# Kernel optimization log

Measured on AMD Instinct MI355X. Metric: run time of the kernel, lower is better.

The kernel has to match this reference:

```python
import jax, jax.numpy as jnp
import numpy as np

N_UE = 16384
N_AP = 128
E = 2097152
D = 32

relu = jax.nn.relu


def setup_inputs():
    key = jax.random.key(0)
    ks = jax.random.split(key, 24)
    def g(i, shape, s=0.1):
        return jax.random.normal(ks[i], shape, dtype=jnp.float32) * s
    inp = {}
    inp["x_ue"] = jax.random.uniform(ks[0], (N_UE, 1), dtype=jnp.float32)
    inp["e_ua"] = g(1, (E, 2), 1.0)
    inp["e_au"] = g(2, (E, 2), 1.0)
    inp["src"] = jax.random.randint(ks[3], (E,), 0, N_UE)
    inp["dst"] = jax.random.randint(ks[4], (E,), 0, N_AP)
    # layer 1 (Ue2Ap): ue feat dim 1, ap feat dim 0, edge dim 2
    inp["Wm1_ua"] = g(5, (1 + 2, D)); inp["bm1_ua"] = jnp.zeros((D,), jnp.float32)
    inp["Wm1_au"] = g(6, (2, D));     inp["bm1_au"] = jnp.zeros((D,), jnp.float32)
    inp["Wu1_ap"] = g(7, (D, D));     inp["bu1_ap"] = jnp.zeros((D,), jnp.float32)
    inp["Wu1_ue"] = g(8, (1 + D, D)); inp["bu1_ue"] = jnp.zeros((D,), jnp.float32)
    inp["We1_ua"] = g(9, (2 * D + 2, 2));  inp["be1_ua"] = jnp.zeros((2,), jnp.float32)
    inp["We1_au"] = g(10, (2 * D + 2, 2)); inp["be1_au"] = jnp.zeros((2,), jnp.float32)
    # layers 2-4 stacked (all 32 -> 32)
    inp["Wm_ua"] = g(11, (3, D + 2, D)); inp["bm_ua"] = jnp.zeros((3, D), jnp.float32)
    inp["Wm_au"] = g(12, (3, D + 2, D)); inp["bm_au"] = jnp.zeros((3, D), jnp.float32)
    inp["Wu_ap"] = g(13, (3, 2 * D, D)); inp["bu_ap"] = jnp.zeros((3, D), jnp.float32)
    inp["Wu_ue"] = g(14, (3, 2 * D, D)); inp["bu_ue"] = jnp.zeros((3, D), jnp.float32)
    inp["We_ua"] = g(15, (3, 2 * D + 2, 2)); inp["be_ua"] = jnp.zeros((3, 2), jnp.float32)
    inp["We_au"] = g(16, (3, 2 * D + 2, 2)); inp["be_au"] = jnp.zeros((3, 2), jnp.float32)
    # power head: mlp([32,16]) + Lin(16,1) + Sigmoid
    inp["Wp1"] = g(17, (D, 16)); inp["bp1"] = jnp.zeros((16,), jnp.float32)
    inp["Wp2"] = g(18, (16, 1)); inp["bp2"] = jnp.zeros((1,), jnp.float32)
    return inp


def _het_conv(x_ue, x_ap, e_ua, e_au, src, dst,
              Wm_ua, bm_ua, Wm_au, bm_au,
              Wu_ap, bu_ap, Wu_ue, bu_ue,
              We_ua, be_ua, We_au, be_au):
    # ue -> ap: gather src ue feats + edge attr, MLP, scatter-add to ap
    f_ua = jnp.concatenate([x_ue[src], e_ua], axis=1)        # [E, d_ue+2]
    m_ua = relu(f_ua @ Wm_ua + bm_ua)                        # [E, D]
    agg_ap = jax.ops.segment_sum(m_ua, dst, num_segments=N_AP)
    # ap -> ue: ap has no features in layer 1 (dim 0)
    f_au = e_au if x_ap is None else jnp.concatenate([x_ap[dst], e_au], axis=1)
    m_au = relu(f_au @ Wm_au + bm_au)                        # [E, D]
    agg_ue = jax.ops.segment_sum(m_au, src, num_segments=N_UE)
    # node updates
    h_ap = agg_ap if x_ap is None else jnp.concatenate([x_ap, agg_ap], axis=1)
    x_ap_new = relu(h_ap @ Wu_ap + bu_ap)                    # [N_AP, D]
    x_ue_new = relu(jnp.concatenate([x_ue, agg_ue], axis=1) @ Wu_ue + bu_ue)  # [N_UE, D]
    # edge updates (keep edge_dim = 2)
    pair = jnp.concatenate([x_ue_new[src], x_ap_new[dst]], axis=1)  # [E, 2D]
    e_ua_new = relu(jnp.concatenate([pair, e_ua], axis=1) @ We_ua + be_ua)
    e_au_new = relu(jnp.concatenate([pair, e_au], axis=1) @ We_au + be_au)
    return x_ue_new, x_ap_new, e_ua_new, e_au_new


def reference(x_ue, e_ua, e_au, src, dst,
              Wm1_ua, bm1_ua, Wm1_au, bm1_au, Wu1_ap, bu1_ap, Wu1_ue, bu1_ue,
              We1_ua, be1_ua, We1_au, be1_au,
              Wm_ua, bm_ua, Wm_au, bm_au, Wu_ap, bu_ap, Wu_ue, bu_ue,
              We_ua, be_ua, We_au, be_au,
              Wp1, bp1, Wp2, bp2):
    x_ue, x_ap, e_ua, e_au = _het_conv(
        x_ue, None, e_ua, e_au, src, dst,
        Wm1_ua, bm1_ua, Wm1_au, bm1_au, Wu1_ap, bu1_ap, Wu1_ue, bu1_ue,
        We1_ua, be1_ua, We1_au, be1_au)
    for l in range(3):  # conv2, conv3, conv4
        x_ue, x_ap, e_ua, e_au = _het_conv(
            x_ue, x_ap, e_ua, e_au, src, dst,
            Wm_ua[l], bm_ua[l], Wm_au[l], bm_au[l],
            Wu_ap[l], bu_ap[l], Wu_ue[l], bu_ue[l],
            We_ua[l], be_ua[l], We_au[l], be_au[l])
    power = jax.nn.sigmoid(relu(x_ue @ Wp1 + bp1) @ Wp2 + bp2)  # [N_UE, 1]
    ue_out = jnp.concatenate([x_ue[:, :1], power], axis=1)      # [N_UE, 2]
    return ue_out, x_ap, e_ua, e_au
```

## Files before the change

### kernel.cpp

```cpp
#include <hip/hip_runtime.h>
#include <math.h>

#define N_UE 16384
#define N_AP 128
#define NE   2097152
#define NSB  256
#define EPSB (NE / NSB)
#define NHALF (N_UE / 2)
#define CHS  8
#define CHD  16
#define NEP  (NE + CHS * N_UE)
#define NCHU (NEP / CHS)
#define NEPD (NE + CHD * N_AP)
#define NCHD_AL 131328
#define SRC_BLKS (NCHU / 256)
#define DST_BLKS (NCHD_AL / 256)

#define RFL(x) __int_as_float(__builtin_amdgcn_readfirstlane(__float_as_int(x)))

__global__ __launch_bounds__(256) void prefill(
    int* __restrict__ dtS, int* __restrict__ srcD,
    int* __restrict__ cnS, int* __restrict__ cnD)
{
    int i = blockIdx.x * 256 + threadIdx.x;
    dtS[i] = N_AP;
    if (i < NEPD) srcD[i] = N_UE;
    if (i < NCHU) cnS[i] = -1;
    if (i < NCHD_AL) cnD[i] = -1;
}

__global__ __launch_bounds__(256) void init_kernel(
    const float* __restrict__ x_ue, const float* __restrict__ Wm1_ua,
    const float* __restrict__ bm1_ua, const float* __restrict__ bm1_au,
    float* __restrict__ Qua, float* __restrict__ Pau)
{
    int i = blockIdx.x * 256 + threadIdx.x;
    int d = i & 31;
    Qua[i] = fmaf(x_ue[i >> 5], Wm1_ua[d], bm1_ua[d]);
    if (i < N_AP * 32) Pau[i] = bm1_au[d];
    if (i < 32) { Qua[N_UE * 32 + i] = -1e30f; Pau[N_AP * 32 + i] = -1e30f; }
}

__global__ __launch_bounds__(256) void hist_both(
    const int* __restrict__ src, const int* __restrict__ dst,
    unsigned short* __restrict__ histS, int* __restrict__ histD)
{
    __shared__ unsigned int h32[N_UE / 2];
    __shared__ int hd[N_AP];
    const int tid = threadIdx.x, b = blockIdx.x;
    for (int i = tid; i < N_UE / 2; i += 256) h32[i] = 0u;
    if (tid < N_AP) hd[tid] = 0;
    __syncthreads();
    const int beg = b * EPSB;
    for (int e = beg + tid; e < beg + EPSB; e += 256) {
        int s = src[e];
        atomicAdd(&h32[s >> 1], 1u << ((s & 1) * 16));
        atomicAdd(&hd[dst[e]], 1);
    }
    __syncthreads();
    for (int i = tid; i < N_UE; i += 256)
        histS[(size_t)b * N_UE + i] =
            (unsigned short)((h32[i >> 1] >> ((i & 1) * 16)) & 0xffffu);
    if (tid < N_AP) histD[b * N_AP + tid] = hd[tid];
}

__global__ __launch_bounds__(256) void colscan_kernel(
    const unsigned short* __restrict__ histS,
    unsigned short* __restrict__ baseS, int* __restrict__ cnt)
{
    const int u = blockIdx.x * 256 + threadIdx.x;
    int run = 0;
    for (int b = 0; b < NSB; ++b) {
        int t = histS[(size_t)b * N_UE + u];
        baseS[(size_t)b * N_UE + u] = (unsigned short)run;
        run += t;
    }
    cnt[u] = run;
}

__global__ __launch_bounds__(256) void scan_src(
    const int* __restrict__ cnt, int* __restrict__ CU)
{
    __shared__ int ps[256];
    __shared__ int ps2[257];
    const int t = threadIdx.x;
    const int b0 = t * (N_UE / 256);
    int s = 0;
    for (int i = 0; i < N_UE / 256; ++i) s += (cnt[b0 + i] + CHS - 1) / CHS;
    ps[t] = s;
    __syncthreads();
    if (t == 0) {
        int r = 0;
        for (int i = 0; i < 256; ++i) { ps2[i] = r; r += ps[i]; }
        ps2[256] = r;
    }
    __syncthreads();
    int r = ps2[t];
    for (int i = 0; i < N_UE / 256; ++i) { CU[b0 + i] = r; r += (cnt[b0 + i] + CHS - 1) / CHS; }
    if (t == 255) CU[N_UE] = ps2[256];
}

__global__ __launch_bounds__(128) void scan_dst(
    const int* __restrict__ histD, int* __restrict__ offsD, int* __restrict__ CA)
{
    __shared__ int colTot[N_AP], colStart[N_AP];
    const int a = threadIdx.x;
    int run = 0;
    for (int b = 0; b < NSB; ++b) {
        offsD[b * N_AP + a] = run;
        run += histD[b * N_AP + a];
    }
    colTot[a] = run;
    __syncthreads();
    if (a == 0) {
        int r = 0;
        for (int i = 0; i < N_AP; ++i) {
            CA[i] = r;
            colStart[i] = r * CHD;
            r += (colTot[i] + CHD - 1) / CHD;
        }
        CA[N_AP] = r;
    }
    __syncthreads();
    const int st = colStart[a];
    for (int b = 0; b < NSB; ++b) offsD[b * N_AP + a] += st;
}

__global__ __launch_bounds__(256) void scatter_both(
    const int* __restrict__ src, const int* __restrict__ dst,
    const float2* __restrict__ e0ua, const float2* __restrict__ e0au,
    const unsigned short* __restrict__ baseS, const int* __restrict__ CU,
    const int* __restrict__ offsD,
    int* __restrict__ dtS, float2* __restrict__ attS, int* __restrict__ invS,
    int* __restrict__ srcD, float2* __restrict__ attD, int* __restrict__ invD)
{
    __shared__ int cursor[NHALF];
    __shared__ int cursord[N_AP];
    const int tid = threadIdx.x, b = blockIdx.x;
    const int beg = b * EPSB;
    if (tid < N_AP) cursord[tid] = offsD[b * N_AP + tid];
    for (int p = 0; p < 2; ++p) {
        const int lo = p * NHALF;
        for (int i = tid; i < NHALF; i += 256)
            cursor[i] = CU[lo + i] * CHS + (int)baseS[(size_t)b * N_UE + lo + i];
        __syncthreads();
        for (int e = beg + tid; e < beg + EPSB; e += 256) {
            int s = src[e];
            int dt = dst[e];
            if (p == 0) {
                int posd = atomicAdd(&cursord[dt], 1);
                srcD[posd] = s;
                attD[posd] = e0ua[e];
                invD[e] = posd;
            }
            if (s >= lo && s < lo + NHALF) {
                int pos = atomicAdd(&cursor[s - lo], 1);
                dtS[pos] = dt;
                attS[pos] = e0au[e];
                invS[e] = pos;
            }
        }
        __syncthreads();
    }
}

__global__ __launch_bounds__(256) void build_map_src(
    const int* __restrict__ CU, int* __restrict__ cnS)
{
    const int u = blockIdx.x * 256 + threadIdx.x;
    const int c0 = CU[u], c1 = CU[u + 1];
    for (int c = c0; c < c1; ++c) cnS[c] = u;
}

__global__ __launch_bounds__(128) void build_map_dst(
    const int* __restrict__ CA, int* __restrict__ cnD)
{
    const int a = threadIdx.x;
    const int c0 = CA[a], c1 = CA[a + 1];
    for (int c = c0; c < c1; ++c) cnD[c] = a;
}

template<bool EUPD>
__global__ __launch_bounds__(256) void pass_both(
    const int* __restrict__ cnS, const int* __restrict__ dtS,
    float2* __restrict__ attS,
    const int* __restrict__ cnD, const int* __restrict__ srcD,
    float2* __restrict__ attD,
    const float2* __restrict__ RueA, const float2* __restrict__ RueB,
    const float2* __restrict__ RapA, const float2* __restrict__ RapB,
    const float* __restrict__ EcA, const float* __restrict__ EcB,
    const float* __restrict__ Qua, const float* __restrict__ Pau,
    const float* __restrict__ cu, const float* __restrict__ cw,
    float* __restrict__ partialU, float* __restrict__ partialA)
{
    if (blockIdx.x < SRC_BLKS) {
        const int ch = blockIdx.x * 256 + threadIdx.x;
        const int u = cnS[ch];
        if (u < 0) return;
        float w0v[32], w1v[32];
        #pragma unroll
        for (int d = 0; d < 32; ++d) { w0v[d] = RFL(cw[d]); w1v[d] = RFL(cw[32 + d]); }
        float d00 = 0.f, d01 = 0.f, d10 = 0.f, d11 = 0.f, rbx = 0.f, rby = 0.f;
        if constexpr (EUPD) {
            d00 = RFL(EcB[0]); d01 = RFL(EcB[1]); d10 = RFL(EcB[2]); d11 = RFL(EcB[3]);
            float2 r = RueB[u]; rbx = r.x; rby = r.y;
        }
        const float4* __restrict__ Pau4 = (const float4*)Pau;
        const int base = ch * CHS;
        float4 acc[8];
        #pragma unroll
        for (int q = 0; q < 8; ++q) acc[q] = make_float4(0.f, 0.f, 0.f, 0.f);
        #pragma unroll
        for (int j = 0; j < CHS; ++j) {
            int dt = dtS[base + j];
            float2 a = attS[base + j];
            if constexpr (EUPD) {
                float2 rp = RapB[dt];
                float m0 = fmaxf(rbx + rp.x + a.x * d00 + a.y * d10, 0.f);
                float m1 = fmaxf(rby + rp.y + a.x * d01 + a.y * d11, 0.f);
                a = make_float2(m0, m1);
                attS[base + j] = a;
            }
            const float4* pr = Pau4 + dt * 8;
            #pragma unroll
            for (int q = 0; q < 8; ++q) {
                float4 pv = pr[q];
                acc[q].x += fmaxf(fmaf(a.x, w0v[q*4+0], fmaf(a.y, w1v[q*4+0], pv.x)), 0.f);
                acc[q].y += fmaxf(fmaf(a.x, w0v[q*4+1], fmaf(a.y, w1v[q*4+1], pv.y)), 0.f);
                acc[q].z += fmaxf(fmaf(a.x, w0v[q*4+2], fmaf(a.y, w1v[q*4+2], pv.z)), 0.f);
                acc[q].w += fmaxf(fmaf(a.x, w0v[q*4+3], fmaf(a.y, w1v[q*4+3], pv.w)), 0.f);
            }
        }
        float4* pu = (float4*)(partialU + (size_t)ch * 32);
        #pragma unroll
        for (int q = 0; q < 8; ++q) pu[q] = acc[q];
    } else {
        const int ch = (blockIdx.x - SRC_BLKS) * 256 + threadIdx.x;
        const int a = cnD[ch];
        if (a < 0) return;
        float u0v[32], u1v[32];
        #pragma unroll
        for (int d = 0; d < 32; ++d) { u0v[d] = RFL(cu[d]); u1v[d] = RFL(cu[32 + d]); }
        float c00 = 0.f, c01 = 0.f, c10 = 0.f, c11 = 0.f, rax = 0.f, ray = 0.f;
        if constexpr (EUPD) {
            c00 = RFL(EcA[0]); c01 = RFL(EcA[1]); c10 = RFL(EcA[2]); c11 = RFL(EcA[3]);
            float2 r = RapA[a]; rax = r.x; ray = r.y;
        }
        const float4* __restrict__ Qua4 = (const float4*)Qua;
        const int base = ch * CHD;
        float4 acc[8];
        #pragma unroll
        for (int q = 0; q < 8; ++q) acc[q] = make_float4(0.f, 0.f, 0.f, 0.f);
        #pragma unroll 4
        for (int j = 0; j < CHD; ++j) {
            int s = srcD[base + j];
            float2 a2 = attD[base + j];
            if constexpr (EUPD) {
                float2 ru = RueA[s];
                float n0 = fmaxf(rax + ru.x + a2.x * c00 + a2.y * c10, 0.f);
                float n1 = fmaxf(ray + ru.y + a2.x * c01 + a2.y * c11, 0.f);
                a2 = make_float2(n0, n1);
                attD[base + j] = a2;
            }
            const float4* qr = Qua4 + s * 8;
            #pragma unroll
            for (int q = 0; q < 8; ++q) {
                float4 qv = qr[q];
                acc[q].x += fmaxf(fmaf(a2.x, u0v[q*4+0], fmaf(a2.y, u1v[q*4+0], qv.x)), 0.f);
                acc[q].y += fmaxf(fmaf(a2.x, u0v[q*4+1], fmaf(a2.y, u1v[q*4+1], qv.y)), 0.f);
                acc[q].z += fmaxf(fmaf(a2.x, u0v[q*4+2], fmaf(a2.y, u1v[q*4+2], qv.z)), 0.f);
                acc[q].w += fmaxf(fmaf(a2.x, u0v[q*4+3], fmaf(a2.y, u1v[q*4+3], qv.w)), 0.f);
            }
        }
        float4* pa = (float4*)(partialA + (size_t)ch * 32);
        #pragma unroll
        for (int q = 0; q < 8; ++q) pa[q] = acc[q];
    }
}

__global__ __launch_bounds__(256) void reduce_ue(
    const int* __restrict__ CU, const float* __restrict__ partialU,
    float* __restrict__ agg_ue)
{
    const int g   = (blockIdx.x * 256 + threadIdx.x) >> 5;
    const int dim = threadIdx.x & 31;
    const int c0 = CU[g], c1 = CU[g + 1];
    float acc = 0.f;
    for (int c = c0; c < c1; ++c) acc += partialU[(size_t)c * 32 + dim];
    agg_ue[g * 32 + dim] = acc;
}

__global__ __launch_bounds__(256) void final_edge(
    const int* __restrict__ src, const int* __restrict__ dst,
    const int* __restrict__ invS, const int* __restrict__ invD,
    const float2* __restrict__ attS, const float2* __restrict__ attD,
    const float2* __restrict__ RueA, const float2* __restrict__ RueB,
    const float2* __restrict__ RapA, const float2* __restrict__ RapB,
    const float* __restrict__ EcA, const float* __restrict__ EcB,
    float2* __restrict__ out_eua, float2* __restrict__ out_eau)
{
    const int e = blockIdx.x * 256 + threadIdx.x;
    const int s = src[e], dt = dst[e];
    float c00 = EcA[0], c01 = EcA[1], c10 = EcA[2], c11 = EcA[3];
    float d00 = EcB[0], d01 = EcB[1], d10 = EcB[2], d11 = EcB[3];
    float2 eua = attD[invD[e]];
    float2 eau = attS[invS[e]];
    float2 rA = RueA[s], pA = RapA[dt];
    float n0 = fmaxf(rA.x + pA.x + eua.x * c00 + eua.y * c10, 0.f);
    float n1 = fmaxf(rA.y + pA.y + eua.x * c01 + eua.y * c11, 0.f);
    float2 rB = RueB[s], pB = RapB[dt];
    float m0 = fmaxf(rB.x + pB.x + eau.x * d00 + eau.y * d10, 0.f);
    float m1 = fmaxf(rB.y + pB.y + eau.x * d01 + eau.y * d11, 0.f);
    out_eua[e] = make_float2(n0, n1);
    out_eau[e] = make_float2(m0, m1);
}

template<bool FIRST, bool LAST>
__global__ __launch_bounds__(64) void node_ue_kernel(
    const float* __restrict__ x_prev, const float* __restrict__ agg_ue,
    const float* __restrict__ Wu, const float* __restrict__ bu,
    const float* __restrict__ Wm_next, const float* __restrict__ bm_next,
    const float* __restrict__ WeUa, const float* __restrict__ WeUb,
    const float* __restrict__ Wp1, const float* __restrict__ bp1,
    const float* __restrict__ Wp2, const float* __restrict__ bp2,
    float* __restrict__ x_new, float* __restrict__ Qua_next,
    float2* __restrict__ RueA, float2* __restrict__ RueB,
    float2* __restrict__ ue_out)
{
    constexpr int KIN = FIRST ? 33 : 64;
    __shared__ float Wu_s[64 * 32];
    __shared__ float Wm_s[32 * 32];
    __shared__ float WeA_s[64], WeB_s[64];
    __shared__ float bu_s[32], bm_s[32];
    __shared__ float Wp1_s[32 * 16], bp1_s[16], Wp2_s[16];

    const int tid = threadIdx.x;
    for (int i = tid; i < KIN * 32; i += 64) Wu_s[i] = Wu[i];
    if (tid < 32) bu_s[tid] = bu[tid];
    if (!LAST) {
        for (int i = tid; i < 1024; i += 64) Wm_s[i] = Wm_next[i];
        if (tid < 32) bm_s[tid] = bm_next[tid];
    }
    { WeA_s[tid] = WeUa[tid]; WeB_s[tid] = WeUb[tid]; }
    if (LAST) {
        for (int i = tid; i < 512; i += 64) Wp1_s[i] = Wp1[i];
        if (tid < 16) { bp1_s[tid] = bp1[tid]; Wp2_s[tid] = Wp2[tid]; }
    }
    __syncthreads();

    const int u = blockIdx.x * 64 + tid;
    float in[KIN];
    if (FIRST) {
        in[0] = x_prev[u];
        #pragma unroll
        for (int k = 0; k < 32; ++k) in[1 + k] = agg_ue[u * 32 + k];
    } else {
        #pragma unroll
        for (int k = 0; k < 32; ++k) in[k] = x_prev[u * 32 + k];
        #pragma unroll
        for (int k = 0; k < 32; ++k) in[32 + k] = agg_ue[u * 32 + k];
    }
    float out[32];
    #pragma unroll
    for (int d = 0; d < 32; ++d) {
        float acc = bu_s[d];
        #pragma unroll
        for (int k = 0; k < KIN; ++k) acc = fmaf(in[k], Wu_s[k * 32 + d], acc);
        out[d] = fmaxf(acc, 0.f);
    }
    #pragma unroll
    for (int d = 0; d < 32; ++d) x_new[u * 32 + d] = out[d];
    if (!LAST) {
        #pragma unroll
        for (int d = 0; d < 32; ++d) {
            float acc = bm_s[d];
            #pragma unroll
            for (int k = 0; k < 32; ++k) acc = fmaf(out[k], Wm_s[k * 32 + d], acc);
            Qua_next[u * 32 + d] = acc;
        }
    }
    float r0 = 0.f, r1 = 0.f, s0 = 0.f, s1 = 0.f;
    #pragma unroll
    for (int k = 0; k < 32; ++k) {
        r0 = fmaf(out[k], WeA_s[k * 2],     r0);
        r1 = fmaf(out[k], WeA_s[k * 2 + 1], r1);
        s0 = fmaf(out[k], WeB_s[k * 2],     s0);
        s1 = fmaf(out[k], WeB_s[k * 2 + 1], s1);
    }
    RueA[u] = make_float2(r0, r1);
    RueB[u] = make_float2(s0, s1);
    if (LAST) {
        float z = bp2[0];
        #pragma unroll
        for (int j = 0; j < 16; ++j) {
            float h = bp1_s[j];
            #pragma unroll
            for (int k = 0; k < 32; ++k) h = fmaf(out[k], Wp1_s[k * 16 + j], h);
// ... 47 lines not shown
        float xn = fmaxf(acc2, 0.f);
        xnew_s[d] = xn;
        x_new[a * 32 + d] = xn;
    }
    __syncthreads();
    if (!LAST) {
        if (tid < 32) {
            float acc3 = bm_next[d];
            #pragma unroll
            for (int k = 0; k < 32; ++k) acc3 = fmaf(xnew_s[k], Wm_next[k * 32 + d], acc3);
            Pau_next[a * 32 + d] = acc3;
        }
    }
    if (tid == 0) {
        float q0 = beA[0], q1 = beA[1], t0 = beB[0], t1 = beB[1];
        #pragma unroll
        for (int k = 0; k < 32; ++k) {
            q0 = fmaf(xnew_s[k], WeA[k * 2],     q0);
            q1 = fmaf(xnew_s[k], WeA[k * 2 + 1], q1);
            t0 = fmaf(xnew_s[k], WeB[k * 2],     t0);
            t1 = fmaf(xnew_s[k], WeB[k * 2 + 1], t1);
        }
        RapA[a] = make_float2(q0, q1);
        RapB[a] = make_float2(t0, t1);
    }
}

extern "C" void kernel_launch(void* const* d_in, const int* in_sizes, int n_in,
                              void* d_out_v, int out_size, void* d_ws, size_t ws_size,
                              hipStream_t stream)
{
    const float*  x_ue   = (const float*)d_in[0];
    const float2* e0ua   = (const float2*)d_in[1];
    const float2* e0au   = (const float2*)d_in[2];
    const int*    src    = (const int*)d_in[3];
    const int*    dst    = (const int*)d_in[4];
    const float* Wm1_ua = (const float*)d_in[5];
    const float* bm1_ua = (const float*)d_in[6];
    const float* Wm1_au = (const float*)d_in[7];
    const float* bm1_au = (const float*)d_in[8];
    const float* Wu1_ap = (const float*)d_in[9];
    const float* bu1_ap = (const float*)d_in[10];
    const float* Wu1_ue = (const float*)d_in[11];
    const float* bu1_ue = (const float*)d_in[12];
    const float* We1_ua = (const float*)d_in[13];
    const float* be1_ua = (const float*)d_in[14];
    const float* We1_au = (const float*)d_in[15];
    const float* be1_au = (const float*)d_in[16];
    const float* Wm_ua  = (const float*)d_in[17];
    const float* bm_ua  = (const float*)d_in[18];
    const float* Wm_au  = (const float*)d_in[19];
    const float* bm_au  = (const float*)d_in[20];
    const float* Wu_ap  = (const float*)d_in[21];
    const float* bu_ap  = (const float*)d_in[22];
    const float* Wu_ue  = (const float*)d_in[23];
    const float* bu_ue  = (const float*)d_in[24];
    const float* We_ua  = (const float*)d_in[25];
    const float* be_ua  = (const float*)d_in[26];
    const float* We_au  = (const float*)d_in[27];
    const float* be_au  = (const float*)d_in[28];
    const float* Wp1    = (const float*)d_in[29];
    const float* bp1    = (const float*)d_in[30];
    const float* Wp2    = (const float*)d_in[31];
    const float* bp2    = (const float*)d_in[32];

    float*  outp    = (float*)d_out_v;
    float2* out_ue  = (float2*)outp;
    float*  out_ap  = outp + N_UE * 2;
    float2* out_eua = (float2*)(outp + N_UE * 2 + N_AP * 32);
    float2* out_eau = (float2*)(outp + N_UE * 2 + N_AP * 32 + (size_t)NE * 2);

    float* ws = (float*)d_ws;
    float* x_ueA  = ws;          ws += N_UE * 32;
    float* x_ueB  = ws;          ws += N_UE * 32;
    float* x_apA  = ws;          ws += N_AP * 32;
    float* x_apB  = ws;          ws += N_AP * 32;
    float* agg_ue = ws;          ws += N_UE * 32;
    float* Qua    = ws;          ws += (N_UE + 1) * 32;
    float* Pau    = ws;          ws += (N_AP + 1) * 32;
    float2* RueA  = (float2*)ws; ws += (N_UE + 2) * 2;
    float2* RueB  = (float2*)ws; ws += (N_UE + 2) * 2;
    float2* RapA  = (float2*)ws; ws += (N_AP + 2) * 2;
    float2* RapB  = (float2*)ws; ws += (N_AP + 2) * 2;
    int* cnt   = (int*)ws;       ws += N_UE;
    int* CU    = (int*)ws;       ws += N_UE + 4;
    int* histD = (int*)ws;       ws += NSB * N_AP;
    int* offsD = (int*)ws;       ws += NSB * N_AP;
    int* CA    = (int*)ws;       ws += N_AP + 4;
    int* cnS   = (int*)ws;       ws += NCHU;
    int* cnD   = (int*)ws;       ws += NCHD_AL;
    int* invS  = (int*)ws;       ws += NE;
    int* invD  = (int*)ws;       ws += NE;
    int* dtS   = (int*)ws;       ws += NEP;
    int* srcD  = (int*)ws;       ws += NEPD;
    float2* attS = (float2*)ws;  ws += (size_t)NEP * 2;
    float2* attD = (float2*)ws;  ws += (size_t)NEPD * 2;
    float* partialU = ws;        ws += (size_t)NCHU * 32;
    float* partialA = ws;        ws += (size_t)NCHD_AL * 32;
    unsigned short* histS = (unsigned short*)partialU;
    unsigned short* baseS = (unsigned short*)(partialU + (size_t)(NSB * N_UE / 2));

    dim3 blk(256);

    prefill<<<NEP / 256, blk, 0, stream>>>(dtS, srcD, cnS, cnD);
    hist_both<<<NSB, blk, 0, stream>>>(src, dst, histS, histD);
    colscan_kernel<<<N_UE / 256, blk, 0, stream>>>(histS, baseS, cnt);
    scan_src<<<1, blk, 0, stream>>>(cnt, CU);
    scan_dst<<<1, dim3(128), 0, stream>>>(histD, offsD, CA);
    scatter_both<<<NSB, blk, 0, stream>>>(src, dst, e0ua, e0au, baseS, CU, offsD,
                                          dtS, attS, invS, srcD, attD, invD);
    build_map_src<<<N_UE / 256, blk, 0, stream>>>(CU, cnS);
    build_map_dst<<<1, dim3(128), 0, stream>>>(CA, cnD);

    init_kernel<<<N_UE * 32 / 256, blk, 0, stream>>>(x_ue, Wm1_ua, bm1_ua, bm1_au, Qua, Pau);

    const int PB = SRC_BLKS + DST_BLKS;

    pass_both<false><<<PB, blk, 0, stream>>>(
        cnS, dtS, attS, cnD, srcD, attD,
        nullptr, nullptr, nullptr, nullptr, nullptr, nullptr,
        Qua, Pau, Wm1_ua + 32, Wm1_au, partialU, partialA);
    reduce_ue<<<N_UE * 32 / 256, blk, 0, stream>>>(CU, partialU, agg_ue);
    node_ue_kernel<true, false><<<N_UE / 64, dim3(64), 0, stream>>>(
        x_ue, agg_ue, Wu1_ue, bu1_ue, Wm_ua, bm_ua, We1_ua, We1_au,
        nullptr, nullptr, nullptr, nullptr,
        x_ueA, Qua, RueA, RueB, nullptr);
    node_ap_kernel<true, false><<<N_AP, blk, 0, stream>>>(
        partialA, CA, nullptr, Wu1_ap, bu1_ap, Wm_au, bm_au,
        We1_ua + 64, be1_ua, We1_au + 64, be1_au,
        x_apA, Pau, RapA, RapB);

    pass_both<true><<<PB, blk, 0, stream>>>(
        cnS, dtS, attS, cnD, srcD, attD,
        RueA, RueB, RapA, RapB, We1_ua + 128, We1_au + 128,
        Qua, Pau, Wm_ua + 1024, Wm_au + 1024, partialU, partialA);
    reduce_ue<<<N_UE * 32 / 256, blk, 0, stream>>>(CU, partialU, agg_ue);
    node_ue_kernel<false, false><<<N_UE / 64, dim3(64), 0, stream>>>(
        x_ueA, agg_ue, Wu_ue, bu_ue, Wm_ua + 1088, bm_ua + 32, We_ua, We_au,
        nullptr, nullptr, nullptr, nullptr,
        x_ueB, Qua, RueA, RueB, nullptr);
    node_ap_kernel<false, false><<<N_AP, blk, 0, stream>>>(
        partialA, CA, x_apA, Wu_ap, bu_ap, Wm_au + 1088, bm_au + 32,
        We_ua + 64, be_ua, We_au + 64, be_au,
        x_apB, Pau, RapA, RapB);

    pass_both<true><<<PB, blk, 0, stream>>>(
        cnS, dtS, attS, cnD, srcD, attD,
        RueA, RueB, RapA, RapB, We_ua + 128, We_au + 128,
        Qua, Pau, Wm_ua + 2112, Wm_au + 2112, partialU, partialA);
    reduce_ue<<<N_UE * 32 / 256, blk, 0, stream>>>(CU, partialU, agg_ue);
    node_ue_kernel<false, false><<<N_UE / 64, dim3(64), 0, stream>>>(
        x_ueB, agg_ue, Wu_ue + 2048, bu_ue + 32, Wm_ua + 2176, bm_ua + 64,
        We_ua + 132, We_au + 132,
        nullptr, nullptr, nullptr, nullptr,
        x_ueA, Qua, RueA, RueB, nullptr);
    node_ap_kernel<false, false><<<N_AP, blk, 0, stream>>>(
        partialA, CA, x_apB, Wu_ap + 2048, bu_ap + 32, Wm_au + 2176, bm_au + 64,
        We_ua + 196, be_ua + 2, We_au + 196, be_au + 2,
        x_apA, Pau, RapA, RapB);

    pass_both<true><<<PB, blk, 0, stream>>>(
        cnS, dtS, attS, cnD, srcD, attD,
        RueA, RueB, RapA, RapB, We_ua + 260, We_au + 260,
        Qua, Pau, Wm_ua + 3200, Wm_au + 3200, partialU, partialA);
    reduce_ue<<<N_UE * 32 / 256, blk, 0, stream>>>(CU, partialU, agg_ue);
    node_ue_kernel<false, true><<<N_UE / 64, dim3(64), 0, stream>>>(
        x_ueA, agg_ue, Wu_ue + 4096, bu_ue + 64, nullptr, nullptr,
        We_ua + 264, We_au + 264,
        Wp1, bp1, Wp2, bp2,
        x_ueB, nullptr, RueA, RueB, out_ue);
    node_ap_kernel<false, true><<<N_AP, blk, 0, stream>>>(
        partialA, CA, x_apA, Wu_ap + 4096, bu_ap + 64, nullptr, nullptr,
        We_ua + 328, be_ua + 4, We_au + 328, be_au + 4,
        out_ap, nullptr, RapA, RapB);

    final_edge<<<NE / 256, blk, 0, stream>>>(
        src, dst, invS, invD, attS, attD,
        RueA, RueB, RapA, RapB,
        We_ua + 392, We_au + 392, out_eua, out_eau);
}
```

Measured before the change: 891.9 us.

## Pack edge records into int4 AoS and scatter final edges by original index

Replaces the separate dst/attr/inverse-index arrays with a single 16-byte record per sorted edge (attr, neighbor, original edge id). The scatter becomes single-pass using packed 16-bit shared counters over all UEs, and NSB doubles while the src chunk size goes from 8 to 16. final_edge now walks the sorted records and writes outputs to the original edge slot, replacing the two indirect gathers through inverse indices with one scattered write. Records are wider, so each pass_both read moves more bytes, and the larger chunk size adds padding.

```diff
diff --git a/kernel.cpp b/kernel.cpp
--- a/kernel.cpp
+++ b/kernel.cpp
@@ -4,10 +4,9 @@
 #define N_UE 16384
 #define N_AP 128
 #define NE   2097152
-#define NSB  256
+#define NSB  512
 #define EPSB (NE / NSB)
-#define NHALF (N_UE / 2)
-#define CHS  8
+#define CHS  16
 #define CHD  16
 #define NEP  (NE + CHS * N_UE)
 #define NCHU (NEP / CHS)
@@ -19,12 +18,12 @@
 #define RFL(x) __int_as_float(__builtin_amdgcn_readfirstlane(__float_as_int(x)))
 
 __global__ __launch_bounds__(256) void prefill(
-    int* __restrict__ dtS, int* __restrict__ srcD,
+    int4* __restrict__ recS, int4* __restrict__ recD,
     int* __restrict__ cnS, int* __restrict__ cnD)
 {
     int i = blockIdx.x * 256 + threadIdx.x;
-    dtS[i] = N_AP;
-    if (i < NEPD) srcD[i] = N_UE;
+    recS[i] = make_int4(0, 0, N_AP, -1);
+    if (i < NEPD) recD[i] = make_int4(0, 0, N_UE, -1);
     if (i < NCHU) cnS[i] = -1;
     if (i < NCHD_AL) cnD[i] = -1;
 }
@@ -131,36 +130,25 @@
     const float2* __restrict__ e0ua, const float2* __restrict__ e0au,
     const unsigned short* __restrict__ baseS, const int* __restrict__ CU,
     const int* __restrict__ offsD,
-    int* __restrict__ dtS, float2* __restrict__ attS, int* __restrict__ invS,
-    int* __restrict__ srcD, float2* __restrict__ attD, int* __restrict__ invD)
-{
-    __shared__ int cursor[NHALF];
-    __shared__ int cursord[N_AP];
+    int4* __restrict__ recS, int4* __restrict__ recD)
+{
+    __shared__ unsigned int curS[N_UE / 2];
+    __shared__ int curD[N_AP];
     const int tid = threadIdx.x, b = blockIdx.x;
+    for (int i = tid; i < N_UE / 2; i += 256) curS[i] = 0u;
+    if (tid < N_AP) curD[tid] = offsD[b * N_AP + tid];
+    __syncthreads();
     const int beg = b * EPSB;
-    if (tid < N_AP) cursord[tid] = offsD[b * N_AP + tid];
-    for (int p = 0; p < 2; ++p) {
-        const int lo = p * NHALF;
-        for (int i = tid; i < NHALF; i += 256)
-            cursor[i] = CU[lo + i] * CHS + (int)baseS[(size_t)b * N_UE + lo + i];
-        __syncthreads();
-        for (int e = beg + tid; e < beg + EPSB; e += 256) {
-            int s = src[e];
-            int dt = dst[e];
-            if (p == 0) {
-                int posd = atomicAdd(&cursord[dt], 1);
-                srcD[posd] = s;
-                attD[posd] = e0ua[e];
-                invD[e] = posd;
-            }
-            if (s >= lo && s < lo + NHALF) {
-                int pos = atomicAdd(&cursor[s - lo], 1);
-                dtS[pos] = dt;
-                attS[pos] = e0au[e];
-                invS[e] = pos;
-            }
-        }
-        __syncthreads();
+    for (int e = beg + tid; e < beg + EPSB; e += 256) {
+        const int s = src[e], dt = dst[e];
+        unsigned int old = atomicAdd(&curS[s >> 1], 1u << ((s & 1) * 16));
+        int local = (int)((old >> ((s & 1) * 16)) & 0xffffu);
+        int pos = CU[s] * CHS + (int)baseS[(size_t)b * N_UE + s] + local;
+        float2 au = e0au[e];
+        recS[pos] = make_int4(__float_as_int(au.x), __float_as_int(au.y), dt, e);
+        int posd = atomicAdd(&curD[dt], 1);
+        float2 ua = e0ua[e];
+        recD[posd] = make_int4(__float_as_int(ua.x), __float_as_int(ua.y), s, e);
     }
 }
 
@@ -182,10 +170,8 @@
 
 template<bool EUPD>
 __global__ __launch_bounds__(256) void pass_both(
-    const int* __restrict__ cnS, const int* __restrict__ dtS,
-    float2* __restrict__ attS,
-    const int* __restrict__ cnD, const int* __restrict__ srcD,
-    float2* __restrict__ attD,
+    const int* __restrict__ cnS, int4* __restrict__ recS,
+    const int* __restrict__ cnD, int4* __restrict__ recD,
     const float2* __restrict__ RueA, const float2* __restrict__ RueB,
     const float2* __restrict__ RapA, const float2* __restrict__ RapB,
     const float* __restrict__ EcA, const float* __restrict__ EcB,
@@ -210,16 +196,17 @@
         float4 acc[8];
         #pragma unroll
         for (int q = 0; q < 8; ++q) acc[q] = make_float4(0.f, 0.f, 0.f, 0.f);
-        #pragma unroll
+        #pragma unroll 4
         for (int j = 0; j < CHS; ++j) {
-            int dt = dtS[base + j];
-            float2 a = attS[base + j];
+            int4 r4 = recS[base + j];
+            int dt = r4.z;
+            float2 a = make_float2(__int_as_float(r4.x), __int_as_float(r4.y));
             if constexpr (EUPD) {
                 float2 rp = RapB[dt];
                 float m0 = fmaxf(rbx + rp.x + a.x * d00 + a.y * d10, 0.f);
                 float m1 = fmaxf(rby + rp.y + a.x * d01 + a.y * d11, 0.f);
                 a = make_float2(m0, m1);
-                attS[base + j] = a;
+                *(float2*)&recS[base + j] = a;
             }
             const float4* pr = Pau4 + dt * 8;
             #pragma unroll
@@ -253,14 +240,15 @@
         for (int q = 0; q < 8; ++q) acc[q] = make_float4(0.f, 0.f, 0.f, 0.f);
         #pragma unroll 4
         for (int j = 0; j < CHD; ++j) {
-            int s = srcD[base + j];
-            float2 a2 = attD[base + j];
+            int4 r4 = recD[base + j];
+            int s = r4.z;
+            float2 a2 = make_float2(__int_as_float(r4.x), __int_as_float(r4.y));
             if constexpr (EUPD) {
                 float2 ru = RueA[s];
                 float n0 = fmaxf(rax + ru.x + a2.x * c00 + a2.y * c10, 0.f);
                 float n1 = fmaxf(ray + ru.y + a2.x * c01 + a2.y * c11, 0.f);
                 a2 = make_float2(n0, n1);
-                attD[base + j] = a2;
+                *(float2*)&recD[base + j] = a2;
             }
             const float4* qr = Qua4 + s * 8;
             #pragma unroll
@@ -291,28 +279,38 @@
 }
 
 __global__ __launch_bounds__(256) void final_edge(
-    const int* __restrict__ src, const int* __restrict__ dst,
-    const int* __restrict__ invS, const int* __restrict__ invD,
-    const float2* __restrict__ attS, const float2* __restrict__ attD,
+    const int4* __restrict__ recS, const int4* __restrict__ recD,
+    const int* __restrict__ cnS, const int* __restrict__ cnD,
     const float2* __restrict__ RueA, const float2* __restrict__ RueB,
     const float2* __restrict__ RapA, const float2* __restrict__ RapB,
     const float* __restrict__ EcA, const float* __restrict__ EcB,
     float2* __restrict__ out_eua, float2* __restrict__ out_eau)
 {
-    const int e = blockIdx.x * 256 + threadIdx.x;
-    const int s = src[e], dt = dst[e];
+    const int i = blockIdx.x * 256 + threadIdx.x;
     float c00 = EcA[0], c01 = EcA[1], c10 = EcA[2], c11 = EcA[3];
     float d00 = EcB[0], d01 = EcB[1], d10 = EcB[2], d11 = EcB[3];
-    float2 eua = attD[invD[e]];
-    float2 eau = attS[invS[e]];
-    float2 rA = RueA[s], pA = RapA[dt];
-    float n0 = fmaxf(rA.x + pA.x + eua.x * c00 + eua.y * c10, 0.f);
-    float n1 = fmaxf(rA.y + pA.y + eua.x * c01 + eua.y * c11, 0.f);
-    float2 rB = RueB[s], pB = RapB[dt];
-    float m0 = fmaxf(rB.x + pB.x + eau.x * d00 + eau.y * d10, 0.f);
-    float m1 = fmaxf(rB.y + pB.y + eau.x * d01 + eau.y * d11, 0.f);
-    out_eua[e] = make_float2(n0, n1);
-    out_eau[e] = make_float2(m0, m1);
+    {
+        int4 r = recS[i];
+        if (r.z != N_AP) {
+            const int u = cnS[i >> 4];
+            float2 a = make_float2(__int_as_float(r.x), __int_as_float(r.y));
+            float2 rB = RueB[u], pB = RapB[r.z];
+            float m0 = fmaxf(rB.x + pB.x + a.x * d00 + a.y * d10, 0.f);
+            float m1 = fmaxf(rB.y + pB.y + a.x * d01 + a.y * d11, 0.f);
+            out_eau[r.w] = make_float2(m0, m1);
+        }
+    }
+    if (i < NEPD) {
+        int4 r = recD[i];
+        if (r.z != N_UE) {
+            const int ap = cnD[i >> 4];
+            float2 a = make_float2(__int_as_float(r.x), __int_as_float(r.y));
+            float2 rA = RueA[r.z], pA = RapA[ap];
+            float n0 = fmaxf(rA.x + pA.x + a.x * c00 + a.y * c10, 0.f);
+            float n1 = fmaxf(rA.y + pA.y + a.x * c01 + a.y * c11, 0.f);
+            out_eua[r.w] = make_float2(n0, n1);
+        }
+    }
 }
 
 template<bool FIRST, bool LAST>
@@ -526,33 +524,29 @@
     float2* RueB  = (float2*)ws; ws += (N_UE + 2) * 2;
     float2* RapA  = (float2*)ws; ws += (N_AP + 2) * 2;
     float2* RapB  = (float2*)ws; ws += (N_AP + 2) * 2;
-    int* cnt   = (int*)ws;       ws += N_UE;
-    int* CU    = (int*)ws;       ws += N_UE + 4;
-    int* histD = (int*)ws;       ws += NSB * N_AP;
-    int* offsD = (int*)ws;       ws += NSB * N_AP;
-    int* CA    = (int*)ws;       ws += N_AP + 4;
-    int* cnS   = (int*)ws;       ws += NCHU;
-    int* cnD   = (int*)ws;       ws += NCHD_AL;
-    int* invS  = (int*)ws;       ws += NE;
-    int* invD  = (int*)ws;       ws += NE;
-    int* dtS   = (int*)ws;       ws += NEP;
-    int* srcD  = (int*)ws;       ws += NEPD;
-    float2* attS = (float2*)ws;  ws += (size_t)NEP * 2;
-    float2* attD = (float2*)ws;  ws += (size_t)NEPD * 2;
+    int* cnt     = (int*)ws;     ws += N_UE;
+    int* CU      = (int*)ws;     ws += N_UE + 4;
+    int* histD   = (int*)ws;     ws += NSB * N_AP;
+    int* offsD   = (int*)ws;     ws += NSB * N_AP;
+    int* CA      = (int*)ws;     ws += N_AP + 4;
+    int* cnS     = (int*)ws;     ws += NCHU;
+    int* cnD     = (int*)ws;     ws += NCHD_AL;
+    int4* recS   = (int4*)ws;    ws += (size_t)NEP * 4;
+    int4* recD   = (int4*)ws;    ws += (size_t)NEPD * 4;
     float* partialU = ws;        ws += (size_t)NCHU * 32;
     float* partialA = ws;        ws += (size_t)NCHD_AL * 32;
     unsigned short* histS = (unsigned short*)partialU;
-    unsigned short* baseS = (unsigned short*)(partialU + (size_t)(NSB * N_UE / 2));
+    unsigned short* baseS = (unsigned short*)partialA;
 
     dim3 blk(256);
 
-    prefill<<<NEP / 256, blk, 0, stream>>>(dtS, srcD, cnS, cnD);
+    prefill<<<NEP / 256, blk, 0, stream>>>(recS, recD, cnS, cnD);
     hist_both<<<NSB, blk, 0, stream>>>(src, dst, histS, histD);
     colscan_kernel<<<N_UE / 256, blk, 0, stream>>>(histS, baseS, cnt);
     scan_src<<<1, blk, 0, stream>>>(cnt, CU);
     scan_dst<<<1, dim3(128), 0, stream>>>(histD, offsD, CA);
     scatter_both<<<NSB, blk, 0, stream>>>(src, dst, e0ua, e0au, baseS, CU, offsD,
-                                          dtS, attS, invS, srcD, attD, invD);
+                                          recS, recD);
     build_map_src<<<N_UE / 256, blk, 0, stream>>>(CU, cnS);
     build_map_dst<<<1, dim3(128), 0, stream>>>(CA, cnD);
 
@@ -561,7 +555,7 @@
     const int PB = SRC_BLKS + DST_BLKS;
 
     pass_both<false><<<PB, blk, 0, stream>>>(
-        cnS, dtS, attS, cnD, srcD, attD,
+        cnS, recS, cnD, recD,
         nullptr, nullptr, nullptr, nullptr, nullptr, nullptr,
         Qua, Pau, Wm1_ua + 32, Wm1_au, partialU, partialA);
     reduce_ue<<<N_UE * 32 / 256, blk, 0, stream>>>(CU, partialU, agg_ue);
@@ -575,7 +569,7 @@
         x_apA, Pau, RapA, RapB);
 
     pass_both<true><<<PB, blk, 0, stream>>>(
-        cnS, dtS, attS, cnD, srcD, attD,
+        cnS, recS, cnD, recD,
         RueA, RueB, RapA, RapB, We1_ua + 128, We1_au + 128,
         Qua, Pau, Wm_ua + 1024, Wm_au + 1024, partialU, partialA);
     reduce_ue<<<N_UE * 32 / 256, blk, 0, stream>>>(CU, partialU, agg_ue);
@@ -589,7 +583,7 @@
         x_apB, Pau, RapA, RapB);
 
     pass_both<true><<<PB, blk, 0, stream>>>(
-        cnS, dtS, attS, cnD, srcD, attD,
+        cnS, recS, cnD, recD,
         RueA, RueB, RapA, RapB, We_ua + 128, We_au + 128,
         Qua, Pau, Wm_ua + 2112, Wm_au + 2112, partialU, partialA);
     reduce_ue<<<N_UE * 32 / 256, blk, 0, stream>>>(CU, partialU, agg_ue);
@@ -604,7 +598,7 @@
         x_apA, Pau, RapA, RapB);
 
     pass_both<true><<<PB, blk, 0, stream>>>(
-        cnS, dtS, attS, cnD, srcD, attD,
+        cnS, recS, cnD, recD,
         RueA, RueB, RapA, RapB, We_ua + 260, We_au + 260,
         Qua, Pau, Wm_ua + 3200, Wm_au + 3200, partialU, partialA);
     reduce_ue<<<N_UE * 32 / 256, blk, 0, stream>>>(CU, partialU, agg_ue);
@@ -618,8 +612,7 @@
         We_ua + 328, be_ua + 4, We_au + 328, be_au + 4,
         out_ap, nullptr, RapA, RapB);
 
-    final_edge<<<NE / 256, blk, 0, stream>>>(
-        src, dst, invS, invD, attS, attD,
-        RueA, RueB, RapA, RapB,
+    final_edge<<<NEP / 256, blk, 0, stream>>>(
+        recS, recD, cnS, cnD, RueA, RueB, RapA, RapB,
         We_ua + 392, We_au + 392, out_eua, out_eau);
 }
```

New measurement: 1.106 ms. 1.24x slower.

## Single-pass packed-cursor scatter, more sort blocks, and larger UE chunks

Applied to the files above, without the earlier changes.

The scatter kernel now writes both sort directions in one pass. It uses packed 16-bit shared-memory cursors for all UEs, which replaces the earlier two-half pass that re-read the edge list. Sort block count and threads per block both double, and the UE chunk size goes from 8 to 16 edges with a partial unroll in the edge pass. The aim is to cut preprocessing traffic and raise per-thread work in the source pass, at the cost of more padding per UE and a relocated baseS buffer.

```diff
diff --git a/kernel.cpp b/kernel.cpp
--- a/kernel.cpp
+++ b/kernel.cpp
@@ -4,10 +4,9 @@
 #define N_UE 16384
 #define N_AP 128
 #define NE   2097152
-#define NSB  256
+#define NSB  512
 #define EPSB (NE / NSB)
-#define NHALF (N_UE / 2)
-#define CHS  8
+#define CHS  16
 #define CHD  16
 #define NEP  (NE + CHS * N_UE)
 #define NCHU (NEP / CHS)
@@ -41,24 +40,24 @@
     if (i < 32) { Qua[N_UE * 32 + i] = -1e30f; Pau[N_AP * 32 + i] = -1e30f; }
 }
 
-__global__ __launch_bounds__(256) void hist_both(
+__global__ __launch_bounds__(512) void hist_both(
     const int* __restrict__ src, const int* __restrict__ dst,
     unsigned short* __restrict__ histS, int* __restrict__ histD)
 {
     __shared__ unsigned int h32[N_UE / 2];
     __shared__ int hd[N_AP];
     const int tid = threadIdx.x, b = blockIdx.x;
-    for (int i = tid; i < N_UE / 2; i += 256) h32[i] = 0u;
+    for (int i = tid; i < N_UE / 2; i += 512) h32[i] = 0u;
     if (tid < N_AP) hd[tid] = 0;
     __syncthreads();
     const int beg = b * EPSB;
-    for (int e = beg + tid; e < beg + EPSB; e += 256) {
+    for (int e = beg + tid; e < beg + EPSB; e += 512) {
         int s = src[e];
         atomicAdd(&h32[s >> 1], 1u << ((s & 1) * 16));
         atomicAdd(&hd[dst[e]], 1);
     }
     __syncthreads();
-    for (int i = tid; i < N_UE; i += 256)
+    for (int i = tid; i < N_UE; i += 512)
         histS[(size_t)b * N_UE + i] =
             (unsigned short)((h32[i >> 1] >> ((i & 1) * 16)) & 0xffffu);
     if (tid < N_AP) histD[b * N_AP + tid] = hd[tid];
@@ -126,7 +125,7 @@
     for (int b = 0; b < NSB; ++b) offsD[b * N_AP + a] += st;
 }
 
-__global__ __launch_bounds__(256) void scatter_both(
+__global__ __launch_bounds__(512) void scatter_both(
     const int* __restrict__ src, const int* __restrict__ dst,
     const float2* __restrict__ e0ua, const float2* __restrict__ e0au,
     const unsigned short* __restrict__ baseS, const int* __restrict__ CU,
@@ -134,33 +133,25 @@
     int* __restrict__ dtS, float2* __restrict__ attS, int* __restrict__ invS,
     int* __restrict__ srcD, float2* __restrict__ attD, int* __restrict__ invD)
 {
-    __shared__ int cursor[NHALF];
-    __shared__ int cursord[N_AP];
+    __shared__ unsigned int curS[N_UE / 2];
+    __shared__ int curD[N_AP];
     const int tid = threadIdx.x, b = blockIdx.x;
+    for (int i = tid; i < N_UE / 2; i += 512) curS[i] = 0u;
+    if (tid < N_AP) curD[tid] = offsD[b * N_AP + tid];
+    __syncthreads();
     const int beg = b * EPSB;
-    if (tid < N_AP) cursord[tid] = offsD[b * N_AP + tid];
-    for (int p = 0; p < 2; ++p) {
-        const int lo = p * NHALF;
-        for (int i = tid; i < NHALF; i += 256)
-            cursor[i] = CU[lo + i] * CHS + (int)baseS[(size_t)b * N_UE + lo + i];
-        __syncthreads();
-        for (int e = beg + tid; e < beg + EPSB; e += 256) {
-            int s = src[e];
-            int dt = dst[e];
-            if (p == 0) {
-                int posd = atomicAdd(&cursord[dt], 1);
-                srcD[posd] = s;
-                attD[posd] = e0ua[e];
-                invD[e] = posd;
-            }
-            if (s >= lo && s < lo + NHALF) {
-                int pos = atomicAdd(&cursor[s - lo], 1);
-                dtS[pos] = dt;
-                attS[pos] = e0au[e];
-                invS[e] = pos;
-            }
-        }
-        __syncthreads();
+    for (int e = beg + tid; e < beg + EPSB; e += 512) {
+        const int s = src[e], dt = dst[e];
+        unsigned int old = atomicAdd(&curS[s >> 1], 1u << ((s & 1) * 16));
+        int local = (int)((old >> ((s & 1) * 16)) & 0xffffu);
+        int pos = CU[s] * CHS + (int)baseS[(size_t)b * N_UE + s] + local;
+        dtS[pos] = dt;
+        attS[pos] = e0au[e];
+        invS[e] = pos;
+        int posd = atomicAdd(&curD[dt], 1);
+        srcD[posd] = s;
+        attD[posd] = e0ua[e];
+        invD[e] = posd;
     }
 }
 
@@ -210,7 +201,7 @@
         float4 acc[8];
         #pragma unroll
         for (int q = 0; q < 8; ++q) acc[q] = make_float4(0.f, 0.f, 0.f, 0.f);
-        #pragma unroll
+        #pragma unroll 4
         for (int j = 0; j < CHS; ++j) {
             int dt = dtS[base + j];
             float2 a = attS[base + j];
@@ -526,33 +517,34 @@
     float2* RueB  = (float2*)ws; ws += (N_UE + 2) * 2;
     float2* RapA  = (float2*)ws; ws += (N_AP + 2) * 2;
     float2* RapB  = (float2*)ws; ws += (N_AP + 2) * 2;
-    int* cnt   = (int*)ws;       ws += N_UE;
-    int* CU    = (int*)ws;       ws += N_UE + 4;
-    int* histD = (int*)ws;       ws += NSB * N_AP;
-    int* offsD = (int*)ws;       ws += NSB * N_AP;
-    int* CA    = (int*)ws;       ws += N_AP + 4;
-    int* cnS   = (int*)ws;       ws += NCHU;
-    int* cnD   = (int*)ws;       ws += NCHD_AL;
-    int* invS  = (int*)ws;       ws += NE;
-    int* invD  = (int*)ws;       ws += NE;
-    int* dtS   = (int*)ws;       ws += NEP;
-    int* srcD  = (int*)ws;       ws += NEPD;
+    int* cnt     = (int*)ws;     ws += N_UE;
+    int* CU      = (int*)ws;     ws += N_UE + 4;
+    int* histD   = (int*)ws;     ws += NSB * N_AP;
+    int* offsD   = (int*)ws;     ws += NSB * N_AP;
+    int* CA      = (int*)ws;     ws += N_AP + 4;
+    int* cnS     = (int*)ws;     ws += NCHU;
+    int* cnD     = (int*)ws;     ws += NCHD_AL;
+    int* invS    = (int*)ws;     ws += NE;
+    int* invD    = (int*)ws;     ws += NE;
+    int* dtS     = (int*)ws;     ws += NEP;
+    int* srcD    = (int*)ws;     ws += NEPD;
     float2* attS = (float2*)ws;  ws += (size_t)NEP * 2;
     float2* attD = (float2*)ws;  ws += (size_t)NEPD * 2;
     float* partialU = ws;        ws += (size_t)NCHU * 32;
     float* partialA = ws;        ws += (size_t)NCHD_AL * 32;
     unsigned short* histS = (unsigned short*)partialU;
-    unsigned short* baseS = (unsigned short*)(partialU + (size_t)(NSB * N_UE / 2));
+    unsigned short* baseS = (unsigned short*)partialA;
 
     dim3 blk(256);
 
     prefill<<<NEP / 256, blk, 0, stream>>>(dtS, srcD, cnS, cnD);
-    hist_both<<<NSB, blk, 0, stream>>>(src, dst, histS, histD);
+    hist_both<<<NSB, dim3(512), 0, stream>>>(src, dst, histS, histD);
     colscan_kernel<<<N_UE / 256, blk, 0, stream>>>(histS, baseS, cnt);
     scan_src<<<1, blk, 0, stream>>>(cnt, CU);
     scan_dst<<<1, dim3(128), 0, stream>>>(histD, offsD, CA);
-    scatter_both<<<NSB, blk, 0, stream>>>(src, dst, e0ua, e0au, baseS, CU, offsD,
-                                          dtS, attS, invS, srcD, attD, invD);
+    scatter_both<<<NSB, dim3(512), 0, stream>>>(src, dst, e0ua, e0au, baseS, CU,
+                                                offsD, dtS, attS, invS,
+                                                srcD, attD, invD);
     build_map_src<<<N_UE / 256, blk, 0, stream>>>(CU, cnS);
     build_map_dst<<<1, dim3(128), 0, stream>>>(CA, cnD);
 
```

Measured after the change: 1.016 ms. 1.14x slower.

## Pack src-sorted edge records into int4 and drop the prefill kernel

Applied to the files above, without the earlier changes.

The separate dtS and attS arrays for the source-sorted edges are merged into one 16-byte record (attr x, attr y, dst, edge id), so each edge in pass_both is fetched with a single vector load. The prefill kernel, which initialised large padding buffers, is removed. Padding slots and unused chunk entries are now filled only where needed inside build_map_src and build_map_dst, which uses the new per-AP counts from scan_dst. The record is 16 bytes instead of 12, so each edge load and store moves more bytes, and the padding fill in build_map is done by serial per-thread loops.

```diff
diff --git a/kernel.cpp b/kernel.cpp
--- a/kernel.cpp
+++ b/kernel.cpp
@@ -18,17 +18,6 @@
 
 #define RFL(x) __int_as_float(__builtin_amdgcn_readfirstlane(__float_as_int(x)))
 
-__global__ __launch_bounds__(256) void prefill(
-    int* __restrict__ dtS, int* __restrict__ srcD,
-    int* __restrict__ cnS, int* __restrict__ cnD)
-{
-    int i = blockIdx.x * 256 + threadIdx.x;
-    dtS[i] = N_AP;
-    if (i < NEPD) srcD[i] = N_UE;
-    if (i < NCHU) cnS[i] = -1;
-    if (i < NCHD_AL) cnD[i] = -1;
-}
-
 __global__ __launch_bounds__(256) void init_kernel(
     const float* __restrict__ x_ue, const float* __restrict__ Wm1_ua,
     const float* __restrict__ bm1_ua, const float* __restrict__ bm1_au,
@@ -101,7 +90,8 @@
 }
 
 __global__ __launch_bounds__(128) void scan_dst(
-    const int* __restrict__ histD, int* __restrict__ offsD, int* __restrict__ CA)
+    const int* __restrict__ histD, int* __restrict__ offsD,
+    int* __restrict__ CA, int* __restrict__ cntD)
 {
     __shared__ int colTot[N_AP], colStart[N_AP];
     const int a = threadIdx.x;
@@ -111,6 +101,7 @@
         run += histD[b * N_AP + a];
     }
     colTot[a] = run;
+    cntD[a] = run;
     __syncthreads();
     if (a == 0) {
         int r = 0;
@@ -131,7 +122,7 @@
     const float2* __restrict__ e0ua, const float2* __restrict__ e0au,
     const unsigned short* __restrict__ baseS, const int* __restrict__ CU,
     const int* __restrict__ offsD,
-    int* __restrict__ dtS, float2* __restrict__ attS, int* __restrict__ invS,
+    int4* __restrict__ recS, int* __restrict__ invS,
     int* __restrict__ srcD, float2* __restrict__ attD, int* __restrict__ invD)
 {
     __shared__ int cursor[NHALF];
@@ -155,8 +146,8 @@
             }
             if (s >= lo && s < lo + NHALF) {
                 int pos = atomicAdd(&cursor[s - lo], 1);
-                dtS[pos] = dt;
-                attS[pos] = e0au[e];
+                float2 au = e0au[e];
+                recS[pos] = make_int4(__float_as_int(au.x), __float_as_int(au.y), dt, e);
                 invS[e] = pos;
             }
         }
@@ -165,25 +156,36 @@
 }
 
 __global__ __launch_bounds__(256) void build_map_src(
-    const int* __restrict__ CU, int* __restrict__ cnS)
+    const int* __restrict__ CU, const int* __restrict__ cnt,
+    int* __restrict__ cnS, int4* __restrict__ recS)
 {
     const int u = blockIdx.x * 256 + threadIdx.x;
     const int c0 = CU[u], c1 = CU[u + 1];
     for (int c = c0; c < c1; ++c) cnS[c] = u;
+    int* recw = (int*)recS;
+    for (int pos = c0 * CHS + cnt[u]; pos < c1 * CHS; ++pos)
+        recw[pos * 4 + 2] = N_AP;
+    const int gid = blockIdx.x * 256 + threadIdx.x;
+    const int cend = CU[N_UE];
+    for (int c = cend + gid; c < NCHU; c += N_UE) cnS[c] = -1;
 }
 
 __global__ __launch_bounds__(128) void build_map_dst(
-    const int* __restrict__ CA, int* __restrict__ cnD)
+    const int* __restrict__ CA, const int* __restrict__ cntD,
+    int* __restrict__ cnD, int* __restrict__ srcD)
 {
     const int a = threadIdx.x;
     const int c0 = CA[a], c1 = CA[a + 1];
     for (int c = c0; c < c1; ++c) cnD[c] = a;
+    for (int pos = c0 * CHD + cntD[a]; pos < c1 * CHD; ++pos)
+        srcD[pos] = N_UE;
+    const int cend = CA[N_AP];
+    for (int c = cend + a; c < NCHD_AL; c += 128) cnD[c] = -1;
 }
 
 template<bool EUPD>
 __global__ __launch_bounds__(256) void pass_both(
-    const int* __restrict__ cnS, const int* __restrict__ dtS,
-    float2* __restrict__ attS,
+    const int* __restrict__ cnS, int4* __restrict__ recS,
     const int* __restrict__ cnD, const int* __restrict__ srcD,
     float2* __restrict__ attD,
     const float2* __restrict__ RueA, const float2* __restrict__ RueB,
@@ -212,14 +214,15 @@
         for (int q = 0; q < 8; ++q) acc[q] = make_float4(0.f, 0.f, 0.f, 0.f);
         #pragma unroll
         for (int j = 0; j < CHS; ++j) {
-            int dt = dtS[base + j];
-            float2 a = attS[base + j];
+            int4 r4 = recS[base + j];
+            int dt = r4.z;
+            float2 a = make_float2(__int_as_float(r4.x), __int_as_float(r4.y));
             if constexpr (EUPD) {
                 float2 rp = RapB[dt];
                 float m0 = fmaxf(rbx + rp.x + a.x * d00 + a.y * d10, 0.f);
                 float m1 = fmaxf(rby + rp.y + a.x * d01 + a.y * d11, 0.f);
                 a = make_float2(m0, m1);
-                attS[base + j] = a;
+                *(float2*)&recS[base + j] = a;
             }
             const float4* pr = Pau4 + dt * 8;
             #pragma unroll
@@ -293,7 +296,7 @@
 __global__ __launch_bounds__(256) void final_edge(
     const int* __restrict__ src, const int* __restrict__ dst,
     const int* __restrict__ invS, const int* __restrict__ invD,
-    const float2* __restrict__ attS, const float2* __restrict__ attD,
+    const int4* __restrict__ recS, const float2* __restrict__ attD,
     const float2* __restrict__ RueA, const float2* __restrict__ RueB,
     const float2* __restrict__ RapA, const float2* __restrict__ RapB,
     const float* __restrict__ EcA, const float* __restrict__ EcB,
@@ -304,7 +307,7 @@
     float c00 = EcA[0], c01 = EcA[1], c10 = EcA[2], c11 = EcA[3];
     float d00 = EcB[0], d01 = EcB[1], d10 = EcB[2], d11 = EcB[3];
     float2 eua = attD[invD[e]];
-    float2 eau = attS[invS[e]];
+    float2 eau = *(const float2*)(recS + invS[e]);
     float2 rA = RueA[s], pA = RapA[dt];
     float n0 = fmaxf(rA.x + pA.x + eua.x * c00 + eua.y * c10, 0.f);
     float n1 = fmaxf(rA.y + pA.y + eua.x * c01 + eua.y * c11, 0.f);
@@ -526,18 +529,18 @@
     float2* RueB  = (float2*)ws; ws += (N_UE + 2) * 2;
     float2* RapA  = (float2*)ws; ws += (N_AP + 2) * 2;
     float2* RapB  = (float2*)ws; ws += (N_AP + 2) * 2;
-    int* cnt   = (int*)ws;       ws += N_UE;
-    int* CU    = (int*)ws;       ws += N_UE + 4;
-    int* histD = (int*)ws;       ws += NSB * N_AP;
-    int* offsD = (int*)ws;       ws += NSB * N_AP;
-    int* CA    = (int*)ws;       ws += N_AP + 4;
-    int* cnS   = (int*)ws;       ws += NCHU;
-    int* cnD   = (int*)ws;       ws += NCHD_AL;
-    int* invS  = (int*)ws;       ws += NE;
-    int* invD  = (int*)ws;       ws += NE;
-    int* dtS   = (int*)ws;       ws += NEP;
-    int* srcD  = (int*)ws;       ws += NEPD;
-    float2* attS = (float2*)ws;  ws += (size_t)NEP * 2;
+    int* cnt     = (int*)ws;     ws += N_UE;
+    int* cntD    = (int*)ws;     ws += N_AP;
+    int* CU      = (int*)ws;     ws += N_UE + 4;
+    int* histD   = (int*)ws;     ws += NSB * N_AP;
+    int* offsD   = (int*)ws;     ws += NSB * N_AP;
+    int* CA      = (int*)ws;     ws += N_AP + 4;
+    int* cnS     = (int*)ws;     ws += NCHU;
+    int* cnD     = (int*)ws;     ws += NCHD_AL;
+    int* invS    = (int*)ws;     ws += NE;
+    int* invD    = (int*)ws;     ws += NE;
+    int4* recS   = (int4*)ws;    ws += (size_t)NEP * 4;
+    int* srcD    = (int*)ws;     ws += NEPD;
     float2* attD = (float2*)ws;  ws += (size_t)NEPD * 2;
     float* partialU = ws;        ws += (size_t)NCHU * 32;
     float* partialA = ws;        ws += (size_t)NCHD_AL * 32;
@@ -546,22 +549,21 @@
 
     dim3 blk(256);
 
-    prefill<<<NEP / 256, blk, 0, stream>>>(dtS, srcD, cnS, cnD);
     hist_both<<<NSB, blk, 0, stream>>>(src, dst, histS, histD);
     colscan_kernel<<<N_UE / 256, blk, 0, stream>>>(histS, baseS, cnt);
     scan_src<<<1, blk, 0, stream>>>(cnt, CU);
-    scan_dst<<<1, dim3(128), 0, stream>>>(histD, offsD, CA);
+    scan_dst<<<1, dim3(128), 0, stream>>>(histD, offsD, CA, cntD);
     scatter_both<<<NSB, blk, 0, stream>>>(src, dst, e0ua, e0au, baseS, CU, offsD,
-                                          dtS, attS, invS, srcD, attD, invD);
-    build_map_src<<<N_UE / 256, blk, 0, stream>>>(CU, cnS);
-    build_map_dst<<<1, dim3(128), 0, stream>>>(CA, cnD);
+                                          recS, invS, srcD, attD, invD);
+    build_map_src<<<N_UE / 256, blk, 0, stream>>>(CU, cnt, cnS, recS);
+    build_map_dst<<<1, dim3(128), 0, stream>>>(CA, cntD, cnD, srcD);
 
     init_kernel<<<N_UE * 32 / 256, blk, 0, stream>>>(x_ue, Wm1_ua, bm1_ua, bm1_au, Qua, Pau);
 
     const int PB = SRC_BLKS + DST_BLKS;
 
     pass_both<false><<<PB, blk, 0, stream>>>(
-        cnS, dtS, attS, cnD, srcD, attD,
+        cnS, recS, cnD, srcD, attD,
         nullptr, nullptr, nullptr, nullptr, nullptr, nullptr,
         Qua, Pau, Wm1_ua + 32, Wm1_au, partialU, partialA);
     reduce_ue<<<N_UE * 32 / 256, blk, 0, stream>>>(CU, partialU, agg_ue);
@@ -575,7 +577,7 @@
         x_apA, Pau, RapA, RapB);
 
     pass_both<true><<<PB, blk, 0, stream>>>(
-        cnS, dtS, attS, cnD, srcD, attD,
+        cnS, recS, cnD, srcD, attD,
         RueA, RueB, RapA, RapB, We1_ua + 128, We1_au + 128,
         Qua, Pau, Wm_ua + 1024, Wm_au + 1024, partialU, partialA);
     reduce_ue<<<N_UE * 32 / 256, blk, 0, stream>>>(CU, partialU, agg_ue);
@@ -589,7 +591,7 @@
         x_apB, Pau, RapA, RapB);
 
     pass_both<true><<<PB, blk, 0, stream>>>(
-        cnS, dtS, attS, cnD, srcD, attD,
+        cnS, recS, cnD, srcD, attD,
         RueA, RueB, RapA, RapB, We_ua + 128, We_au + 128,
         Qua, Pau, Wm_ua + 2112, Wm_au + 2112, partialU, partialA);
     reduce_ue<<<N_UE * 32 / 256, blk, 0, stream>>>(CU, partialU, agg_ue);
@@ -604,7 +606,7 @@
         x_apA, Pau, RapA, RapB);
 
     pass_both<true><<<PB, blk, 0, stream>>>(
-        cnS, dtS, attS, cnD, srcD, attD,
+        cnS, recS, cnD, srcD, attD,
         RueA, RueB, RapA, RapB, We_ua + 260, We_au + 260,
         Qua, Pau, Wm_ua + 3200, Wm_au + 3200, partialU, partialA);
     reduce_ue<<<N_UE * 32 / 256, blk, 0, stream>>>(CU, partialU, agg_ue);
@@ -619,7 +621,7 @@
         out_ap, nullptr, RapA, RapB);
 
     final_edge<<<NE / 256, blk, 0, stream>>>(
-        src, dst, invS, invD, attS, attD,
+        src, dst, invS, invD, recS, attD,
         RueA, RueB, RapA, RapB,
         We_ua + 392, We_au + 392, out_eua, out_eau);
 }
```

Result: slower. 919.9 us (+3.1%).
